# Performance work log

Hardware: AMD Instinct MI355X
Metric: run time of the kernel (lower is better)

Reference implementation:

```python
import jax, jax.numpy as jnp
import numpy as np
from jax import lax

MAX_DISP = 4  # max_displacement; kernel_size = 1


def setup_inputs() -> dict:
    key = jax.random.key(0)
    k1, k2 = jax.random.split(key)
    B, C, H, W = 8, 96, 160, 320
    in1 = jax.random.normal(k1, (B, C, H, W), dtype=jnp.float32)
    in2 = jax.random.normal(k2, (B, C, H, W), dtype=jnp.float32)
    return {"in1": in1, "in2": in2}


def reference(in1, in2):
    """FlowNet/PWC-Net correlation layer, kernel_size=1, max_displacement=4.

    out[b, w, y, x] = mean_c in1[b, c, y, x] * in2[b, c, y+dy, x+dx]
    with zero padding outside, dy = w // 9 - 4, dx = w % 9 - 4
    (matches the torch unfold window ordering).
    """
    pad = MAX_DISP
    B, C, H, W = in1.shape
    in2p = jnp.pad(in2, ((0, 0), (0, 0), (pad, pad), (pad, pad)))
    outs = []
    # fixed 9x9 displacement grid (81 slices) -- not a data-dim loop
    for dy in range(-pad, pad + 1):
        for dx in range(-pad, pad + 1):
            shifted = lax.dynamic_slice(
                in2p, (0, 0, pad + dy, pad + dx), (B, C, H, W)
            )
            outs.append(jnp.mean(in1 * shifted, axis=1))  # [B, H, W]
    return jnp.stack(outs, axis=1)  # [B, 81, H, W]
```

## Files before the change

### kernel.cpp

```cpp
#include <hip/hip_runtime.h>


#define BB 8
#define CC 96
#define HH 160
#define WW 320
#define TY 8
#define TX 64
#define CK 8
#define S1W 68
#define S2W 76
#define NT 576

__global__ __launch_bounds__(NT, 2)
void corr_kernel(const float* __restrict__ in1,
                 const float* __restrict__ in2,
                 float* __restrict__ out) {
    const int x0 = blockIdx.x * TX;
    const int y0 = blockIdx.y * TY;
    const int b  = blockIdx.z;

    const int tid  = threadIdx.x;
    const int dy   = tid >> 6;
    const int lane = tid & 63;
    const int yi   = lane >> 3;
    const int xt   = lane & 7;

    __shared__ float s1[CK][TY][S1W];
    __shared__ float s2[CK][TY + 8][S2W];

    float acc[9][8];
#pragma unroll
    for (int i = 0; i < 9; ++i)
#pragma unroll
        for (int j = 0; j < 8; ++j) acc[i][j] = 0.0f;

    for (int c0 = 0; c0 < CC; c0 += CK) {
        __syncthreads();
        for (int i = tid; i < CK * TY * (TX / 4); i += NT) {
            const int k   = i >> 7;
            const int rem = i & 127;
            const int yy  = rem >> 4;
            const int xg  = rem & 15;
            const float4 v = *reinterpret_cast<const float4*>(
                in1 + (((b * CC + c0 + k) * HH + y0 + yy) * WW + x0 + 4 * xg));
            *reinterpret_cast<float4*>(&s1[k][yy][4 * xg]) = v;
        }
        for (int i = tid; i < CK * (TY + 8) * 18; i += NT) {
            const int k   = i / ((TY + 8) * 18);
            const int rem = i % ((TY + 8) * 18);
            const int r   = rem / 18;
            const int xg  = rem % 18;
            const int yy  = y0 + r - 4;
            const int xs  = x0 - 4 + 4 * xg;
            float4 v = make_float4(0.f, 0.f, 0.f, 0.f);
            if ((unsigned)yy < HH && (unsigned)xs <= (WW - 4)) {
                v = *reinterpret_cast<const float4*>(
                    in2 + (((b * CC + c0 + k) * HH + yy) * WW + xs));
            }
            *reinterpret_cast<float4*>(&s2[k][r][4 * xg]) = v;
        }
        __syncthreads();

#pragma unroll
        for (int k = 0; k < CK; ++k) {
            float a[8];
            *reinterpret_cast<float4*>(&a[0]) =
                *reinterpret_cast<const float4*>(&s1[k][yi][8 * xt]);
            *reinterpret_cast<float4*>(&a[4]) =
                *reinterpret_cast<const float4*>(&s1[k][yi][8 * xt + 4]);
            float v[16];
#pragma unroll
            for (int q = 0; q < 4; ++q)
                *reinterpret_cast<float4*>(&v[4 * q]) =
                    *reinterpret_cast<const float4*>(&s2[k][yi + dy][8 * xt + 4 * q]);
#pragma unroll
            for (int dxi = 0; dxi < 9; ++dxi)
#pragma unroll
                for (int xi = 0; xi < 8; ++xi)
                    acc[dxi][xi] = fmaf(a[xi], v[xi + dxi], acc[dxi][xi]);
        }
    }

    const float scale = 1.0f / (float)CC;
#pragma unroll
    for (int dxi = 0; dxi < 9; ++dxi) {
        float4 o0 = make_float4(acc[dxi][0] * scale, acc[dxi][1] * scale,
                                acc[dxi][2] * scale, acc[dxi][3] * scale);
        float4 o1 = make_float4(acc[dxi][4] * scale, acc[dxi][5] * scale,
                                acc[dxi][6] * scale, acc[dxi][7] * scale);
        float* dst = out +
            (((b * 81 + dy * 9 + dxi) * HH + y0 + yi) * WW + x0 + 8 * xt);
        *reinterpret_cast<float4*>(dst)     = o0;
        *reinterpret_cast<float4*>(dst + 4) = o1;
    }
}

extern "C" void kernel_launch(void* const* d_in, const int* in_sizes, int n_in,
                              void* d_out, int out_size, void* d_ws, size_t ws_size,
                              hipStream_t stream) {
    const float* in1 = (const float*)d_in[0];
    const float* in2 = (const float*)d_in[1];
    float* out = (float*)d_out;
    dim3 grid(WW / TX, HH / TY, BB);
    corr_kernel<<<grid, NT, 0, stream>>>(in1, in2, out);
}
```

Before: 302.9 us.

## Register-prefetch next channel chunk to overlap global loads with compute

Global-to-shared loads now go through registers, and the next channel chunk is fetched right after the barrier so those loads overlap with the FMA loop on the current chunk. Load addresses are computed once outside the loop instead of with per-iteration div/mod. Launch bounds drop from two blocks per CU to one, which allows more registers per thread but may lower occupancy. The lane-to-(y,x) mapping is also swapped, which changes the LDS access pattern and the coalescing of the output stores.

```diff
diff --git a/kernel.cpp b/kernel.cpp
--- a/kernel.cpp
+++ b/kernel.cpp
@@ -8,11 +8,13 @@
 #define TY 8
 #define TX 64
 #define CK 8
+#define NCH (CC / CK)
 #define S1W 68
 #define S2W 76
 #define NT 576
+#define HWSZ (HH * WW)
 
-__global__ __launch_bounds__(NT, 2)
+__global__ __launch_bounds__(NT, 1)
 void corr_kernel(const float* __restrict__ in1,
                  const float* __restrict__ in2,
                  float* __restrict__ out) {
@@ -23,11 +25,47 @@
     const int tid  = threadIdx.x;
     const int dy   = tid >> 6;
     const int lane = tid & 63;
-    const int yi   = lane >> 3;
-    const int xt   = lane & 7;
+    const int yi   = lane & 7;
+    const int xt   = lane >> 3;
 
     __shared__ float s1[CK][TY][S1W];
     __shared__ float s2[CK][TY + 8][S2W];
+
+    const float* g1a;
+    float4* l1a;
+    {
+        const int i = tid, k = i >> 7, rem = i & 127, yy = rem >> 4, xg = rem & 15;
+        g1a = in1 + ((b * CC + k) * HH + y0 + yy) * WW + x0 + 4 * xg;
+        l1a = (float4*)&s1[k][yy][4 * xg];
+    }
+    const bool has1b = (tid < 448);
+    const float* g1b = in1;
+    float4* l1b = (float4*)&s1[0][0][0];
+    if (has1b) {
+        const int i = tid + NT, k = i >> 7, rem = i & 127, yy = rem >> 4, xg = rem & 15;
+        g1b = in1 + ((b * CC + k) * HH + y0 + yy) * WW + x0 + 4 * xg;
+        l1b = (float4*)&s1[k][yy][4 * xg];
+    }
+    const float* g2[4];
+    float4* l2[4];
+    bool ok2[4];
+#pragma unroll
+    for (int j = 0; j < 4; ++j) {
+        const int i = tid + j * NT;
+        const int k = i / 288, rem = i % 288, r = rem / 18, xg = rem % 18;
+        const int yy = y0 + r - 4, xs = x0 - 4 + 4 * xg;
+        ok2[j] = ((unsigned)yy < (unsigned)HH) && ((unsigned)xs <= (unsigned)(WW - 4));
+        g2[j] = in2 + ((b * CC + k) * HH + (ok2[j] ? yy : 0)) * WW + (ok2[j] ? xs : 0);
+        l2[j] = (float4*)&s2[k][r][4 * xg];
+    }
+
+    const float4 z4 = make_float4(0.f, 0.f, 0.f, 0.f);
+    float4 p1a, p1b, p2[4];
+
+    p1a = *(const float4*)g1a;
+    p1b = has1b ? *(const float4*)g1b : z4;
+#pragma unroll
+    for (int j = 0; j < 4; ++j) p2[j] = ok2[j] ? *(const float4*)g2[j] : z4;
 
     float acc[9][8];
 #pragma unroll
@@ -35,45 +73,31 @@
 #pragma unroll
         for (int j = 0; j < 8; ++j) acc[i][j] = 0.0f;
 
-    for (int c0 = 0; c0 < CC; c0 += CK) {
+    for (int ch = 0; ch < NCH; ++ch) {
         __syncthreads();
-        for (int i = tid; i < CK * TY * (TX / 4); i += NT) {
-            const int k   = i >> 7;
-            const int rem = i & 127;
-            const int yy  = rem >> 4;
-            const int xg  = rem & 15;
-            const float4 v = *reinterpret_cast<const float4*>(
-                in1 + (((b * CC + c0 + k) * HH + y0 + yy) * WW + x0 + 4 * xg));
-            *reinterpret_cast<float4*>(&s1[k][yy][4 * xg]) = v;
+        *l1a = p1a;
+        if (has1b) *l1b = p1b;
+#pragma unroll
+        for (int j = 0; j < 4; ++j) *l2[j] = p2[j];
+        __syncthreads();
+
+        if (ch + 1 < NCH) {
+            const int coff = (ch + 1) * CK * HWSZ;
+            p1a = *(const float4*)(g1a + coff);
+            if (has1b) p1b = *(const float4*)(g1b + coff);
+#pragma unroll
+            for (int j = 0; j < 4; ++j)
+                p2[j] = ok2[j] ? *(const float4*)(g2[j] + coff) : z4;
         }
-        for (int i = tid; i < CK * (TY + 8) * 18; i += NT) {
-            const int k   = i / ((TY + 8) * 18);
-            const int rem = i % ((TY + 8) * 18);
-            const int r   = rem / 18;
-            const int xg  = rem % 18;
-            const int yy  = y0 + r - 4;
-            const int xs  = x0 - 4 + 4 * xg;
-            float4 v = make_float4(0.f, 0.f, 0.f, 0.f);
-            if ((unsigned)yy < HH && (unsigned)xs <= (WW - 4)) {
-                v = *reinterpret_cast<const float4*>(
-                    in2 + (((b * CC + c0 + k) * HH + yy) * WW + xs));
-            }
-            *reinterpret_cast<float4*>(&s2[k][r][4 * xg]) = v;
-        }
-        __syncthreads();
 
 #pragma unroll
         for (int k = 0; k < CK; ++k) {
-            float a[8];
-            *reinterpret_cast<float4*>(&a[0]) =
-                *reinterpret_cast<const float4*>(&s1[k][yi][8 * xt]);
-            *reinterpret_cast<float4*>(&a[4]) =
-                *reinterpret_cast<const float4*>(&s1[k][yi][8 * xt + 4]);
-            float v[16];
+            float a[8], v[16];
+            *(float4*)&a[0] = *(const float4*)&s1[k][yi][8 * xt];
+            *(float4*)&a[4] = *(const float4*)&s1[k][yi][8 * xt + 4];
 #pragma unroll
             for (int q = 0; q < 4; ++q)
-                *reinterpret_cast<float4*>(&v[4 * q]) =
-                    *reinterpret_cast<const float4*>(&s2[k][yi + dy][8 * xt + 4 * q]);
+                *(float4*)&v[4 * q] = *(const float4*)&s2[k][yi + dy][8 * xt + 4 * q];
 #pragma unroll
             for (int dxi = 0; dxi < 9; ++dxi)
 #pragma unroll
@@ -91,8 +115,8 @@
                                 acc[dxi][6] * scale, acc[dxi][7] * scale);
         float* dst = out +
             (((b * 81 + dy * 9 + dxi) * HH + y0 + yi) * WW + x0 + 8 * xt);
-        *reinterpret_cast<float4*>(dst)     = o0;
-        *reinterpret_cast<float4*>(dst + 4) = o1;
+        *(float4*)dst       = o0;
+        *(float4*)(dst + 4) = o1;
     }
 }
 
```

Result: slower. 528.4 us (+74.4%).

## Halve tile width, load in1 directly, precompute in2 slots, raise occupancy

Applied to the files above, without the earlier changes.

Narrows the x tile to 32 so each thread holds 4 outputs per displacement, cutting registers and allowing four blocks per CU. in1 is read directly from global memory instead of being staged in shared memory. in2 load addresses and bounds checks are computed once, and zero padding is written only once. The trade-off is a larger halo fraction for in2 and repeated in1 reads across the nine dy groups.

```diff
diff --git a/kernel.cpp b/kernel.cpp
--- a/kernel.cpp
+++ b/kernel.cpp
@@ -6,13 +6,17 @@
 #define HH 160
 #define WW 320
 #define TY 8
-#define TX 64
+#define TX 32
 #define CK 8
-#define S1W 68
-#define S2W 76
+#define NCH (CC / CK)
+#define HR (TY + 8)
+#define SW 44
 #define NT 576
+#define HW (HH * WW)
+#define NSLOT (CK * HR * (SW / 4))
+#define NSTG 3
 
-__global__ __launch_bounds__(NT, 2)
+__global__ __launch_bounds__(NT, 4)
 void corr_kernel(const float* __restrict__ in1,
                  const float* __restrict__ in2,
                  float* __restrict__ out) {
@@ -26,58 +30,63 @@
     const int yi   = lane >> 3;
     const int xt   = lane & 7;
 
-    __shared__ float s1[CK][TY][S1W];
-    __shared__ float s2[CK][TY + 8][S2W];
+    __shared__ __align__(16) float s2[CK][HR][SW];
 
-    float acc[9][8];
+    int goff[NSTG];
+    float4* lsl[NSTG];
+    bool ok[NSTG];
+#pragma unroll
+    for (int t = 0; t < NSTG; ++t) {
+        const int i = tid + t * NT;
+        ok[t] = false; goff[t] = 0; lsl[t] = (float4*)&s2[0][0][0];
+        if (i < NSLOT) {
+            const int k = i / (HR * 11), rem = i % (HR * 11);
+            const int r = rem / 11, c4 = rem % 11;
+            lsl[t] = (float4*)&s2[k][r][4 * c4];
+            const int yy = y0 + r - 4;
+            const int xs = x0 - 4 + 4 * c4;
+            if (c4 < 10 && (unsigned)yy < (unsigned)HH &&
+                (unsigned)xs <= (unsigned)(WW - 4)) {
+                ok[t] = true;
+                goff[t] = (k * HH + yy) * WW + xs;
+            }
+        }
+    }
+
+    {
+        const float4 z = make_float4(0.f, 0.f, 0.f, 0.f);
+        float4* p = (float4*)&s2[0][0][0];
+        for (int i = tid; i < NSLOT; i += NT) p[i] = z;
+    }
+
+    float acc[9][4];
 #pragma unroll
     for (int i = 0; i < 9; ++i)
 #pragma unroll
-        for (int j = 0; j < 8; ++j) acc[i][j] = 0.0f;
+        for (int j = 0; j < 4; ++j) acc[i][j] = 0.0f;
 
-    for (int c0 = 0; c0 < CC; c0 += CK) {
+    const float* in1p = in1 + ((size_t)(b * CC) * HH + y0 + yi) * WW + x0 + 4 * xt;
+
+    for (int ch = 0; ch < NCH; ++ch) {
+        const int cb = (b * CC + ch * CK) * HW;
         __syncthreads();
-        for (int i = tid; i < CK * TY * (TX / 4); i += NT) {
-            const int k   = i >> 7;
-            const int rem = i & 127;
-            const int yy  = rem >> 4;
-            const int xg  = rem & 15;
-            const float4 v = *reinterpret_cast<const float4*>(
-                in1 + (((b * CC + c0 + k) * HH + y0 + yy) * WW + x0 + 4 * xg));
-            *reinterpret_cast<float4*>(&s1[k][yy][4 * xg]) = v;
-        }
-        for (int i = tid; i < CK * (TY + 8) * 18; i += NT) {
-            const int k   = i / ((TY + 8) * 18);
-            const int rem = i % ((TY + 8) * 18);
-            const int r   = rem / 18;
-            const int xg  = rem % 18;
-            const int yy  = y0 + r - 4;
-            const int xs  = x0 - 4 + 4 * xg;
-            float4 v = make_float4(0.f, 0.f, 0.f, 0.f);
-            if ((unsigned)yy < HH && (unsigned)xs <= (WW - 4)) {
-                v = *reinterpret_cast<const float4*>(
-                    in2 + (((b * CC + c0 + k) * HH + yy) * WW + xs));
-            }
-            *reinterpret_cast<float4*>(&s2[k][r][4 * xg]) = v;
-        }
+#pragma unroll
+        for (int t = 0; t < NSTG; ++t)
+            if (ok[t]) *lsl[t] = *(const float4*)(in2 + cb + goff[t]);
         __syncthreads();
 
 #pragma unroll
         for (int k = 0; k < CK; ++k) {
-            float a[8];
-            *reinterpret_cast<float4*>(&a[0]) =
-                *reinterpret_cast<const float4*>(&s1[k][yi][8 * xt]);
-            *reinterpret_cast<float4*>(&a[4]) =
-                *reinterpret_cast<const float4*>(&s1[k][yi][8 * xt + 4]);
-            float v[16];
+            float a[4];
+            *(float4*)a = *(const float4*)(in1p + (size_t)(ch * CK + k) * HW);
+            float v[12];
 #pragma unroll
-            for (int q = 0; q < 4; ++q)
-                *reinterpret_cast<float4*>(&v[4 * q]) =
-                    *reinterpret_cast<const float4*>(&s2[k][yi + dy][8 * xt + 4 * q]);
+            for (int q = 0; q < 3; ++q)
+                *(float4*)&v[4 * q] = *(const float4*)&s2[k][yi + dy][4 * xt + 4 * q];
 #pragma unroll
             for (int dxi = 0; dxi < 9; ++dxi)
 #pragma unroll
-                for (int xi = 0; xi < 8; ++xi)
+                for (int xi = 0; xi < 4; ++xi)
                     acc[dxi][xi] = fmaf(a[xi], v[xi + dxi], acc[dxi][xi]);
         }
     }
@@ -85,14 +94,11 @@
     const float scale = 1.0f / (float)CC;
 #pragma unroll
     for (int dxi = 0; dxi < 9; ++dxi) {
-        float4 o0 = make_float4(acc[dxi][0] * scale, acc[dxi][1] * scale,
-                                acc[dxi][2] * scale, acc[dxi][3] * scale);
-        float4 o1 = make_float4(acc[dxi][4] * scale, acc[dxi][5] * scale,
-                                acc[dxi][6] * scale, acc[dxi][7] * scale);
+        float4 o = make_float4(acc[dxi][0] * scale, acc[dxi][1] * scale,
+                               acc[dxi][2] * scale, acc[dxi][3] * scale);
         float* dst = out +
-            (((b * 81 + dy * 9 + dxi) * HH + y0 + yi) * WW + x0 + 8 * xt);
-        *reinterpret_cast<float4*>(dst)     = o0;
-        *reinterpret_cast<float4*>(dst + 4) = o1;
+            (((size_t)(b * 81 + dy * 9 + dxi) * HH + y0 + yi) * WW + x0 + 4 * xt);
+        *(float4*)dst = o;
     }
 }
 
```

New measurement: 305.2 us. No clear change (+0.8%).
